# Performance work log

Hardware: AMD Instinct MI355X
Metric: run time of the kernel (lower is better)

Reference implementation:

```python
import jax, jax.numpy as jnp
import numpy as np

N_NODES = 100000
N_FEATS = 256
OUT_DIM = 64
NNZ_X = 1280000
N_EDGES = 1600000
KEEP_PROB = 0.9  # 1 - dropout_rate (dropout_rate = 0.1)


def setup_inputs() -> dict:
    key = jax.random.key(0)
    ks = jax.random.split(key, 7)
    feat_values = jax.random.normal(ks[0], (NNZ_X,), dtype=jnp.float32)
    feat_rows = jax.random.randint(ks[1], (NNZ_X,), 0, N_NODES, dtype=jnp.int32)
    feat_cols = jax.random.randint(ks[2], (NNZ_X,), 0, N_FEATS, dtype=jnp.int32)
    # GlorotNormal kernel: std = sqrt(2 / (fan_in + fan_out))
    glorot_std = float(np.sqrt(2.0 / (N_FEATS + OUT_DIM)))
    kernel = jax.random.normal(ks[3], (N_FEATS, OUT_DIM), dtype=jnp.float32) * glorot_std
    adj_values = jax.random.uniform(ks[4], (N_EDGES,), dtype=jnp.float32)
    adj_rows = jax.random.randint(ks[5], (N_EDGES,), 0, N_NODES, dtype=jnp.int32)
    adj_cols = jax.random.randint(ks[6], (N_EDGES,), 0, N_NODES, dtype=jnp.int32)
    return {
        "feat_values": feat_values,
        "kernel": kernel,
        "adj_values": adj_values,
        "feat_rows": feat_rows,
        "feat_cols": feat_cols,
        "adj_rows": adj_rows,
        "adj_cols": adj_cols,
    }


def reference(feat_values, kernel, adj_values, feat_rows, feat_cols, adj_rows, adj_cols):
    # sparse dropout on feature values (training=True path), deterministic key.
    # tf: keep = floor(keep_prob + U[0,1)) cast to bool; retain then scale 1/keep_prob
    u = jax.random.uniform(jax.random.key(42), feat_values.shape, dtype=feat_values.dtype)
    keep = jnp.floor(KEEP_PROB + u).astype(bool)
    v = jnp.where(keep, feat_values, jnp.zeros_like(feat_values)) * (1.0 / KEEP_PROB)

    # SpMM 1: XW[n, o] = sum_{(n,f) in X} v * kernel[f, o]
    xw = jax.ops.segment_sum(v[:, None] * kernel[feat_cols], feat_rows,
                             num_segments=N_NODES)  # [N, OUT]

    # SpMM 2: out[i, o] = sum_{(i,j) in A} a_ij * xw[j, o]
    agg = jax.ops.segment_sum(adj_values[:, None] * xw[adj_cols], adj_rows,
                              num_segments=N_NODES)  # [N, OUT]

    return jax.nn.relu(agg)
```

## Files before the change

### kernel.cpp

```cpp
#include <hip/hip_runtime.h>

#define N_NODES 100000
#define N_FEATS 256
#define OUT_DIM 64
#define NNZ_X   1280000
#define N_EDGES 1600000
#define NB      391
#define CHUNK   4096
#define KPT     8
#define CAPX    4352
#define CAPA    5120

__device__ __forceinline__ unsigned rotl32(unsigned x, unsigned d) {
    return (x << d) | (x >> (32u - d));
}

__device__ __forceinline__ float jax_uniform_42(unsigned e) {
    unsigned x0 = 0u, x1 = e;
    const unsigned ks0 = 0u, ks1 = 42u, ks2 = 0u ^ 42u ^ 0x1BD11BDAu;
    x0 += ks0; x1 += ks1;
#define TF_R(r) { x0 += x1; x1 = rotl32(x1, r); x1 ^= x0; }
    TF_R(13) TF_R(15) TF_R(26) TF_R(6)
    x0 += ks1; x1 += ks2 + 1u;
    TF_R(17) TF_R(29) TF_R(16) TF_R(24)
    x0 += ks2; x1 += ks0 + 2u;
    TF_R(13) TF_R(15) TF_R(26) TF_R(6)
    x0 += ks0; x1 += ks1 + 3u;
    TF_R(17) TF_R(29) TF_R(16) TF_R(24)
    x0 += ks1; x1 += ks2 + 4u;
    TF_R(13) TF_R(15) TF_R(26) TF_R(6)
    x0 += ks2; x1 += ks0 + 5u;
#undef TF_R
    unsigned bits = x0 ^ x1;
    return __uint_as_float((bits >> 9) | 0x3f800000u) - 1.0f;
}

__device__ __forceinline__ bool keep_42(unsigned e) {
    float u = jax_uniform_42(e);
    return floorf(0.9f + u) != 0.0f;
}

__device__ __forceinline__ unsigned short f32_bf16(float f) {
    unsigned bits = __float_as_uint(f);
    return (unsigned short)((bits + 0x7fffu + ((bits >> 16) & 1u)) >> 16);
}

__device__ __forceinline__ float bf16_f32(unsigned short u) {
    return __uint_as_float((unsigned)u << 16);
}

__global__ __launch_bounds__(512) void phase1(
        const float* __restrict__ fvals, const int* __restrict__ frows,
        const int* __restrict__ fcols,
        const float* __restrict__ avals, const int* __restrict__ arows,
        const int* __restrict__ acols,
        int* __restrict__ bcur_x, int* __restrict__ bcur_a,
        float2* __restrict__ gx, float2* __restrict__ ga) {
    const int isA = blockIdx.y;
    const float* vals = isA ? avals : fvals;
    const int* rows   = isA ? arows : frows;
    const int* cols   = isA ? acols : fcols;
    int* bcur         = isA ? bcur_a : bcur_x;
    float2* dst       = isA ? ga : gx;
    const unsigned cap = isA ? CAPA : CAPX;
    const unsigned n  = isA ? N_EDGES : NNZ_X;

    unsigned t = threadIdx.x;
    unsigned base = blockIdx.x * CHUNK;
    if (base >= n) return;

    __shared__ int cnt[512];
    __shared__ int start[512];
    __shared__ int cur[512];
    __shared__ int gbase[NB];
    __shared__ int s[256];
    __shared__ unsigned pArr[CHUNK];

    int rcache[KPT];

    cnt[t] = 0;
    __syncthreads();
    #pragma unroll
    for (int k = 0; k < KPT; k++) {
        unsigned i = base + k * 512u + t;
        int r = -1;
        if (i < n) {
            int rr = rows[i];
            if (isA || keep_42(i)) r = rr;
        }
        rcache[k] = r;
        if (r >= 0) atomicAdd(&cnt[(unsigned)r >> 8], 1);
    }
    __syncthreads();
    if (t < 256) s[t] = cnt[2*t] + cnt[2*t+1];
    __syncthreads();
    for (int off = 1; off < 256; off <<= 1) {
        int v = (t < 256u && t >= (unsigned)off) ? s[t - off] : 0;
        __syncthreads();
        if (t < 256u) s[t] += v;
        __syncthreads();
    }
    if (t < 256u) {
        int excl = t ? s[t-1] : 0;
        start[2*t]   = excl;
        start[2*t+1] = excl + cnt[2*t];
        cur[2*t]     = excl;
        cur[2*t+1]   = excl + cnt[2*t];
    }
    for (unsigned b = t; b < NB; b += 512u) {
        int cb = cnt[b];
        if (cb > 0) gbase[b] = atomicAdd(&bcur[b], cb);
    }
    __syncthreads();
    int n_valid = s[255];
    #pragma unroll
    for (int k = 0; k < KPT; k++) {
        int r = rcache[k];
        if (r >= 0) {
            unsigned b = (unsigned)r >> 8;
            int p = atomicAdd(&cur[b], 1);
            pArr[p] = (b << 20) | (((unsigned)r & 255u) << 12) | (k * 512u + t);
        }
    }
    __syncthreads();
    #pragma unroll
    for (int k = 0; k < KPT; k++) {
        int sidx = k * 512 + (int)t;
        if (sidx < n_valid) {
            unsigned m = pArr[sidx];
            unsigned b = m >> 20;
            unsigned rowlow = (m >> 12) & 255u;
            unsigned i = base + (m & 4095u);
            float v = vals[i];
            if (!isA) v *= (float)(1.0 / 0.9);
            unsigned packed = ((unsigned)cols[i] << 8) | rowlow;
            float2 e; e.x = v; e.y = __int_as_float((int)packed);
            dst[(size_t)b * cap + gbase[b] + (sidx - start[b])] = e;
        }
    }
}

__global__ __launch_bounds__(512) void sort_stage(
        const int* __restrict__ bcur_x, const float2* __restrict__ gx,
        const float* __restrict__ W, unsigned short* __restrict__ xw,
        const int* __restrict__ bcur_a, float2* __restrict__ ga,
        unsigned short* __restrict__ rs) {
    __shared__ float2 ent[CAPX];
    __shared__ int hist[256];
    __shared__ int starts[256];
    __shared__ int cursor[256];
    __shared__ int wtot[4];
    unsigned t = threadIdx.x;
    unsigned wid = t >> 6, lane = t & 63u;
    const int isA = (blockIdx.x >= NB);
    unsigned b = isA ? (blockIdx.x - NB) : blockIdx.x;

    if (!isA) {
        int cnt = bcur_x[b];
        const float2* src = gx + (size_t)b * CAPX;
        if (t < 256) hist[t] = 0;
        __syncthreads();
        for (int i = (int)t; i < cnt; i += 512)
            atomicAdd(&hist[((unsigned)__float_as_int(src[i].y)) & 255u], 1);
        __syncthreads();
        int inc = 0, binv = 0;
        if (wid < 4u) {
            unsigned bin = wid * 64u + lane;
            binv = hist[bin];
            inc = binv;
            #pragma unroll
            for (int d = 1; d < 64; d <<= 1) {
                int v = __shfl_up(inc, d, 64);
                if (lane >= (unsigned)d) inc += v;
            }
            if (lane == 63u) wtot[wid] = inc;
        }
        __syncthreads();
        if (wid < 4u) {
            int offw = 0;
            #pragma unroll
            for (int w = 0; w < 4; w++) if ((unsigned)w < wid) offw += wtot[w];
            unsigned bin = wid * 64u + lane;
            int excl = inc - binv + offw;
            starts[bin] = excl;
            cursor[bin] = excl;
        }
        __syncthreads();
        for (int i = (int)t; i < cnt; i += 512) {
            float2 e = src[i];
            int pos = atomicAdd(&cursor[((unsigned)__float_as_int(e.y)) & 255u], 1);
            ent[pos] = e;
        }
        __syncthreads();
        unsigned quarter = lane >> 4, sub = lane & 15u;
        const float4* W4 = (const float4*)W;
        ushort4* xw4 = (ushort4*)xw;
        for (unsigned r = wid; r < 256u; r += 8u) {
            int s0 = starts[r];
            int s1 = (r == 255u) ? cnt : starts[r + 1];
            float4 acc[4];
            #pragma unroll
            for (int j = 0; j < 4; j++) { acc[j].x = acc[j].y = acc[j].z = acc[j].w = 0.0f; }
            int p = s0;
            for (; p + 16 <= s1; p += 16) {
                float2 e[4];
                #pragma unroll
                for (int j = 0; j < 4; j++) e[j] = ent[p + 4 * quarter + j];
                float4 w[4];
                #pragma unroll
                for (int j = 0; j < 4; j++)
                    w[j] = W4[(((unsigned)__float_as_int(e[j].y)) >> 8) * 16u + sub];
                #pragma unroll
                for (int j = 0; j < 4; j++) {
                    acc[j].x = fmaf(e[j].x, w[j].x, acc[j].x);
                    acc[j].y = fmaf(e[j].x, w[j].y, acc[j].y);
                    acc[j].z = fmaf(e[j].x, w[j].z, acc[j].z);
                    acc[j].w = fmaf(e[j].x, w[j].w, acc[j].w);
                }
            }
            for (int q = p + (int)quarter; q < s1; q += 4) {
                float2 e = ent[q];
                float4 w = W4[(((unsigned)__float_as_int(e.y)) >> 8) * 16u + sub];
                acc[0].x = fmaf(e.x, w.x, acc[0].x);
                acc[0].y = fmaf(e.x, w.y, acc[0].y);
                acc[0].z = fmaf(e.x, w.z, acc[0].z);
                acc[0].w = fmaf(e.x, w.w, acc[0].w);
            }
            float ax = (acc[0].x + acc[1].x) + (acc[2].x + acc[3].x);
            float ay = (acc[0].y + acc[1].y) + (acc[2].y + acc[3].y);
            float az = (acc[0].z + acc[1].z) + (acc[2].z + acc[3].z);
            float aw = (acc[0].w + acc[1].w) + (acc[2].w + acc[3].w);
            ax += __shfl(ax, (int)(lane ^ 16u), 64);
            ay += __shfl(ay, (int)(lane ^ 16u), 64);
            az += __shfl(az, (int)(lane ^ 16u), 64);
            aw += __shfl(aw, (int)(lane ^ 16u), 64);
            ax += __shfl(ax, (int)(lane ^ 32u), 64);
            ay += __shfl(ay, (int)(lane ^ 32u), 64);
            az += __shfl(az, (int)(lane ^ 32u), 64);
            aw += __shfl(aw, (int)(lane ^ 32u), 64);
            unsigned grow = (b << 8) + r;
            if (quarter == 0 && grow < N_NODES) {
                ushort4 o;
                o.x = f32_bf16(ax); o.y = f32_bf16(ay);
                o.z = f32_bf16(az); o.w = f32_bf16(aw);
                xw4[(size_t)grow * 16u + sub] = o;
            }
        }
    } else {
        int cnt = bcur_a[b];
        float2* g = ga + (size_t)b * CAPA;
        if (t < 256) hist[t] = 0;
        __syncthreads();
        float2 ec[10];
        #pragma unroll
        for (int k = 0; k < 10; k++) {
            int i = k * 512 + (int)t;
            if (i < cnt) {
                float2 e = g[i];
                ec[k] = e;
                atomicAdd(&hist[((unsigned)__float_as_int(e.y)) & 255u], 1);
            }
        }
        __syncthreads();
        int inc = 0, binv = 0;
        if (wid < 4u) {
            unsigned bin = wid * 64u + lane;
            binv = hist[bin];
            inc = binv;
            #pragma unroll
            for (int d = 1; d < 64; d <<= 1) {
                int v = __shfl_up(inc, d, 64);
                if (lane >= (unsigned)d) inc += v;
            }
            if (lane == 63u) wtot[wid] = inc;
        }
        __syncthreads();
        if (wid < 4u) {
            int offw = 0;
            #pragma unroll
            for (int w = 0; w < 4; w++) if ((unsigned)w < wid) offw += wtot[w];
            unsigned bin = wid * 64u + lane;
            int excl = inc - binv + offw;
            cursor[bin] = excl;
            rs[(b << 8) + bin] = (unsigned short)excl;
        }
        __syncthreads();
        #pragma unroll
        for (int k = 0; k < 10; k++) {
            int i = k * 512 + (int)t;
            if (i < cnt) {
                unsigned packed = (unsigned)__float_as_int(ec[k].y);
                int pos = atomicAdd(&cursor[packed & 255u], 1);
                float2 o; o.x = ec[k].x; o.y = __int_as_float((int)(packed >> 8));
                g[pos] = o;
            }
        }
    }
}

__global__ void spmm2(const int* __restrict__ bcur_a,
                      const unsigned short* __restrict__ rs_a,
                      const float2* __restrict__ ga,
                      const unsigned short* __restrict__ xw,
                      float* __restrict__ out) {
    unsigned row  = blockIdx.x * 4u + (threadIdx.x >> 6);
    unsigned lane = threadIdx.x & 63u;
    if (row >= N_NODES) return;
    unsigned b = row >> 8, rl = row & 255u;
    int cnt = bcur_a[b];
    const float2* ent = ga + (size_t)b * CAPA;
    int s0 = rs_a[row];
    int s1 = (rl == 255u) ? cnt : (int)rs_a[row + 1];
    unsigned quarter = lane >> 4;
    unsigned sub     = lane & 15u;
    const ushort4* xw4 = (const ushort4*)xw;

    float4 acc[4];
    #pragma unroll
    for (int j = 0; j < 4; j++) { acc[j].x = acc[j].y = acc[j].z = acc[j].w = 0.0f; }
    int p = s0;
    for (; p + 16 <= s1; p += 16) {
        float2 e[4];
        #pragma unroll
        for (int j = 0; j < 4; j++) e[j] = ent[p + 4 * quarter + j];
        ushort4 u[4];
        #pragma unroll
        for (int j = 0; j < 4; j++)
            u[j] = xw4[((unsigned)__float_as_int(e[j].y)) * 16u + sub];
        #pragma unroll
        for (int j = 0; j < 4; j++) {
            acc[j].x = fmaf(e[j].x, bf16_f32(u[j].x), acc[j].x);
            acc[j].y = fmaf(e[j].x, bf16_f32(u[j].y), acc[j].y);
            acc[j].z = fmaf(e[j].x, bf16_f32(u[j].z), acc[j].z);
            acc[j].w = fmaf(e[j].x, bf16_f32(u[j].w), acc[j].w);
        }
    }
    for (int q = p + (int)quarter; q < s1; q += 4) {
        float2 e = ent[q];
        ushort4 u = xw4[((unsigned)__float_as_int(e.y)) * 16u + sub];
        acc[0].x = fmaf(e.x, bf16_f32(u.x), acc[0].x);
        acc[0].y = fmaf(e.x, bf16_f32(u.y), acc[0].y);
        acc[0].z = fmaf(e.x, bf16_f32(u.z), acc[0].z);
        acc[0].w = fmaf(e.x, bf16_f32(u.w), acc[0].w);
    }
    float ax = (acc[0].x + acc[1].x) + (acc[2].x + acc[3].x);
    float ay = (acc[0].y + acc[1].y) + (acc[2].y + acc[3].y);
    float az = (acc[0].z + acc[1].z) + (acc[2].z + acc[3].z);
    float aw = (acc[0].w + acc[1].w) + (acc[2].w + acc[3].w);
    ax += __shfl(ax, (int)(lane ^ 16u), 64);
    ay += __shfl(ay, (int)(lane ^ 16u), 64);
    az += __shfl(az, (int)(lane ^ 16u), 64);
    aw += __shfl(aw, (int)(lane ^ 16u), 64);
    ax += __shfl(ax, (int)(lane ^ 32u), 64);
    ay += __shfl(ay, (int)(lane ^ 32u), 64);
    az += __shfl(az, (int)(lane ^ 32u), 64);
    aw += __shfl(aw, (int)(lane ^ 32u), 64);
    if (quarter == 0) {
        float4 o;
        o.x = fmaxf(ax, 0.0f);
        o.y = fmaxf(ay, 0.0f);
        o.z = fmaxf(az, 0.0f);
        o.w = fmaxf(aw, 0.0f);
        ((float4*)out)[(size_t)row * 16u + sub] = o;
    }
}

extern "C" void kernel_launch(void* const* d_in, const int* in_sizes, int n_in,
                              void* d_out, int out_size, void* d_ws, size_t ws_size,
                              hipStream_t stream) {
    const float* feat_values = (const float*)d_in[0];
    const float* W           = (const float*)d_in[1];
    const float* adj_values  = (const float*)d_in[2];
    const int*   feat_rows   = (const int*)d_in[3];
    const int*   feat_cols   = (const int*)d_in[4];
    const int*   adj_rows    = (const int*)d_in[5];
    const int*   adj_cols    = (const int*)d_in[6];
    float* out = (float*)d_out;

    char* ws = (char*)d_ws;
    int* bcur_x = (int*)(ws + 0);
    int* bcur_a = (int*)(ws + 2048);
    unsigned short* rs_a = (unsigned short*)(ws + 4096);
    float2* gx  = (float2*)(ws + 204800);
    float2* ga  = (float2*)(ws + 13817856);
    unsigned short* xw = (unsigned short*)(ws + 29833216);

    hipMemsetAsync(ws, 0, 4096, stream);

    dim3 gp1((N_EDGES + CHUNK - 1) / CHUNK, 2);
    phase1<<<gp1, 512, 0, stream>>>(feat_values, feat_rows, feat_cols,
                                    adj_values, adj_rows, adj_cols,
                                    bcur_x, bcur_a, gx, ga);
    sort_stage<<<2 * NB, 512, 0, stream>>>(bcur_x, gx, W, xw, bcur_a, ga, rs_a);
    spmm2<<<(N_NODES + 3) / 4, 256, 0, stream>>>(bcur_a, rs_a, ga, xw, out);
}
```

Before: 209.7 us.

## Halve phase1 chunk, use wave-shuffle scan, process two rows per wave in spmm2

Phase1 now handles 2048 entries per block with 4 per thread and replaces the barrier-heavy shared-memory Hillis-Steele scan with a wave-level shuffle scan plus per-wave totals. The spmm2 kernel assigns two adjacent rows to each wavefront and interleaves their gathers, giving more independent loads in flight per wave. The intent is fewer block barriers and more memory-level parallelism. The cost is more blocks and global atomics in phase1, and higher register pressure and some load imbalance in spmm2.

```diff
diff --git a/kernel.cpp b/kernel.cpp
--- a/kernel.cpp
+++ b/kernel.cpp
@@ -6,8 +6,8 @@
 #define NNZ_X   1280000
 #define N_EDGES 1600000
 #define NB      391
-#define CHUNK   4096
-#define KPT     8
+#define CHUNK   2048
+#define KPT     4
 #define CAPX    4352
 #define CAPA    5120
 
@@ -66,6 +66,7 @@
     const unsigned n  = isA ? N_EDGES : NNZ_X;
 
     unsigned t = threadIdx.x;
+    unsigned wid = t >> 6, lane = t & 63u;
     unsigned base = blockIdx.x * CHUNK;
     if (base >= n) return;
 
@@ -73,7 +74,7 @@
     __shared__ int start[512];
     __shared__ int cur[512];
     __shared__ int gbase[NB];
-    __shared__ int s[256];
+    __shared__ int wtot[8];
     __shared__ unsigned pArr[CHUNK];
 
     int rcache[KPT];
@@ -92,27 +93,28 @@
         if (r >= 0) atomicAdd(&cnt[(unsigned)r >> 8], 1);
     }
     __syncthreads();
-    if (t < 256) s[t] = cnt[2*t] + cnt[2*t+1];
+    int binv = cnt[t];
+    int inc = binv;
+    #pragma unroll
+    for (int d = 1; d < 64; d <<= 1) {
+        int v = __shfl_up(inc, d, 64);
+        if (lane >= (unsigned)d) inc += v;
+    }
+    if (lane == 63u) wtot[wid] = inc;
     __syncthreads();
-    for (int off = 1; off < 256; off <<= 1) {
-        int v = (t < 256u && t >= (unsigned)off) ? s[t - off] : 0;
-        __syncthreads();
-        if (t < 256u) s[t] += v;
-        __syncthreads();
-    }
-    if (t < 256u) {
-        int excl = t ? s[t-1] : 0;
-        start[2*t]   = excl;
-        start[2*t+1] = excl + cnt[2*t];
-        cur[2*t]     = excl;
-        cur[2*t+1]   = excl + cnt[2*t];
-    }
-    for (unsigned b = t; b < NB; b += 512u) {
-        int cb = cnt[b];
-        if (cb > 0) gbase[b] = atomicAdd(&bcur[b], cb);
-    }
+    int offw = 0, total = 0;
+    #pragma unroll
+    for (int w = 0; w < 8; w++) {
+        int wv = wtot[w];
+        if ((unsigned)w < wid) offw += wv;
+        total += wv;
+    }
+    int excl = inc - binv + offw;
+    start[t] = excl;
+    cur[t]   = excl;
+    if (t < NB && binv > 0) gbase[t] = atomicAdd(&bcur[t], binv);
     __syncthreads();
-    int n_valid = s[255];
+    int n_valid = total;
     #pragma unroll
     for (int k = 0; k < KPT; k++) {
         int r = rcache[k];
@@ -130,7 +132,7 @@
             unsigned m = pArr[sidx];
             unsigned b = m >> 20;
             unsigned rowlow = (m >> 12) & 255u;
-            unsigned i = base + (m & 4095u);
+            unsigned i = base + (m & 2047u);
             float v = vals[i];
             if (!isA) v *= (float)(1.0 / 0.9);
             unsigned packed = ((unsigned)cols[i] << 8) | rowlow;
@@ -303,65 +305,137 @@
                       const float2* __restrict__ ga,
                       const unsigned short* __restrict__ xw,
                       float* __restrict__ out) {
-    unsigned row  = blockIdx.x * 4u + (threadIdx.x >> 6);
+    unsigned wid  = threadIdx.x >> 6;
     unsigned lane = threadIdx.x & 63u;
-    if (row >= N_NODES) return;
-    unsigned b = row >> 8, rl = row & 255u;
+    unsigned pair = blockIdx.x * 4u + wid;
+    unsigned row0 = pair * 2u;
+    if (row0 >= N_NODES) return;
+    unsigned row1 = row0 + 1u;
+    unsigned b = row0 >> 8;
     int cnt = bcur_a[b];
     const float2* ent = ga + (size_t)b * CAPA;
-    int s0 = rs_a[row];
-    int s1 = (rl == 255u) ? cnt : (int)rs_a[row + 1];
+    int s0a = rs_a[row0];
+    int s1a = rs_a[row1];
+    int s0b = s1a;
+    unsigned rl1 = row1 & 255u;
+    int s1b = (rl1 == 255u) ? cnt : (int)rs_a[row1 + 1];
     unsigned quarter = lane >> 4;
     unsigned sub     = lane & 15u;
     const ushort4* xw4 = (const ushort4*)xw;
 
-    float4 acc[4];
-    #pragma unroll
-    for (int j = 0; j < 4; j++) { acc[j].x = acc[j].y = acc[j].z = acc[j].w = 0.0f; }
-    int p = s0;
-    for (; p + 16 <= s1; p += 16) {
+    float4 accA[4], accB[4];
+    #pragma unroll
+    for (int j = 0; j < 4; j++) {
+        accA[j].x = accA[j].y = accA[j].z = accA[j].w = 0.0f;
+        accB[j].x = accB[j].y = accB[j].z = accB[j].w = 0.0f;
+    }
+    int pa = s0a, pb = s0b;
+    while (pa + 16 <= s1a && pb + 16 <= s1b) {
+        float2 ea[4], eb[4];
+        #pragma unroll
+        for (int j = 0; j < 4; j++) {
+            ea[j] = ent[pa + 4 * quarter + j];
+            eb[j] = ent[pb + 4 * quarter + j];
+        }
+        ushort4 ua[4], ub[4];
+        #pragma unroll
+        for (int j = 0; j < 4; j++) {
+            ua[j] = xw4[((unsigned)__float_as_int(ea[j].y)) * 16u + sub];
+            ub[j] = xw4[((unsigned)__float_as_int(eb[j].y)) * 16u + sub];
+        }
+        #pragma unroll
+        for (int j = 0; j < 4; j++) {
+            accA[j].x = fmaf(ea[j].x, bf16_f32(ua[j].x), accA[j].x);
+            accA[j].y = fmaf(ea[j].x, bf16_f32(ua[j].y), accA[j].y);
+            accA[j].z = fmaf(ea[j].x, bf16_f32(ua[j].z), accA[j].z);
+            accA[j].w = fmaf(ea[j].x, bf16_f32(ua[j].w), accA[j].w);
+            accB[j].x = fmaf(eb[j].x, bf16_f32(ub[j].x), accB[j].x);
+            accB[j].y = fmaf(eb[j].x, bf16_f32(ub[j].y), accB[j].y);
+            accB[j].z = fmaf(eb[j].x, bf16_f32(ub[j].z), accB[j].z);
+            accB[j].w = fmaf(eb[j].x, bf16_f32(ub[j].w), accB[j].w);
+        }
+        pa += 16; pb += 16;
+    }
+    for (; pa + 16 <= s1a; pa += 16) {
         float2 e[4];
         #pragma unroll
-        for (int j = 0; j < 4; j++) e[j] = ent[p + 4 * quarter + j];
+        for (int j = 0; j < 4; j++) e[j] = ent[pa + 4 * quarter + j];
         ushort4 u[4];
         #pragma unroll
         for (int j = 0; j < 4; j++)
             u[j] = xw4[((unsigned)__float_as_int(e[j].y)) * 16u + sub];
         #pragma unroll
         for (int j = 0; j < 4; j++) {
-            acc[j].x = fmaf(e[j].x, bf16_f32(u[j].x), acc[j].x);
-            acc[j].y = fmaf(e[j].x, bf16_f32(u[j].y), acc[j].y);
-            acc[j].z = fmaf(e[j].x, bf16_f32(u[j].z), acc[j].z);
-            acc[j].w = fmaf(e[j].x, bf16_f32(u[j].w), acc[j].w);
-        }
-    }
-    for (int q = p + (int)quarter; q < s1; q += 4) {
+            accA[j].x = fmaf(e[j].x, bf16_f32(u[j].x), accA[j].x);
+            accA[j].y = fmaf(e[j].x, bf16_f32(u[j].y), accA[j].y);
+            accA[j].z = fmaf(e[j].x, bf16_f32(u[j].z), accA[j].z);
+            accA[j].w = fmaf(e[j].x, bf16_f32(u[j].w), accA[j].w);
+        }
+    }
+    for (int q = pa + (int)quarter; q < s1a; q += 4) {
         float2 e = ent[q];
         ushort4 u = xw4[((unsigned)__float_as_int(e.y)) * 16u + sub];
-        acc[0].x = fmaf(e.x, bf16_f32(u.x), acc[0].x);
-        acc[0].y = fmaf(e.x, bf16_f32(u.y), acc[0].y);
-        acc[0].z = fmaf(e.x, bf16_f32(u.z), acc[0].z);
-        acc[0].w = fmaf(e.x, bf16_f32(u.w), acc[0].w);
-    }
-    float ax = (acc[0].x + acc[1].x) + (acc[2].x + acc[3].x);
-    float ay = (acc[0].y + acc[1].y) + (acc[2].y + acc[3].y);
-    float az = (acc[0].z + acc[1].z) + (acc[2].z + acc[3].z);
-    float aw = (acc[0].w + acc[1].w) + (acc[2].w + acc[3].w);
+        accA[0].x = fmaf(e.x, bf16_f32(u.x), accA[0].x);
+        accA[0].y = fmaf(e.x, bf16_f32(u.y), accA[0].y);
+        accA[0].z = fmaf(e.x, bf16_f32(u.z), accA[0].z);
+        accA[0].w = fmaf(e.x, bf16_f32(u.w), accA[0].w);
+    }
+    for (; pb + 16 <= s1b; pb += 16) {
+        float2 e[4];
+        #pragma unroll
+        for (int j = 0; j < 4; j++) e[j] = ent[pb + 4 * quarter + j];
+        ushort4 u[4];
+        #pragma unroll
+        for (int j = 0; j < 4; j++)
+            u[j] = xw4[((unsigned)__float_as_int(e[j].y)) * 16u + sub];
+        #pragma unroll
+        for (int j = 0; j < 4; j++) {
+            accB[j].x = fmaf(e[j].x, bf16_f32(u[j].x), accB[j].x);
+            accB[j].y = fmaf(e[j].x, bf16_f32(u[j].y), accB[j].y);
+            accB[j].z = fmaf(e[j].x, bf16_f32(u[j].z), accB[j].z);
+            accB[j].w = fmaf(e[j].x, bf16_f32(u[j].w), accB[j].w);
+        }
+    }
+    for (int q = pb + (int)quarter; q < s1b; q += 4) {
+        float2 e = ent[q];
+        ushort4 u = xw4[((unsigned)__float_as_int(e.y)) * 16u + sub];
+        accB[0].x = fmaf(e.x, bf16_f32(u.x), accB[0].x);
+        accB[0].y = fmaf(e.x, bf16_f32(u.y), accB[0].y);
+        accB[0].z = fmaf(e.x, bf16_f32(u.z), accB[0].z);
+        accB[0].w = fmaf(e.x, bf16_f32(u.w), accB[0].w);
+    }
+    float ax = (accA[0].x + accA[1].x) + (accA[2].x + accA[3].x);
+    float ay = (accA[0].y + accA[1].y) + (accA[2].y + accA[3].y);
+    float az = (accA[0].z + accA[1].z) + (accA[2].z + accA[3].z);
+    float aw = (accA[0].w + accA[1].w) + (accA[2].w + accA[3].w);
+    float bx = (accB[0].x + accB[1].x) + (accB[2].x + accB[3].x);
+    float by = (accB[0].y + accB[1].y) + (accB[2].y + accB[3].y);
+    float bz = (accB[0].z + accB[1].z) + (accB[2].z + accB[3].z);
+    float bw = (accB[0].w + accB[1].w) + (accB[2].w + accB[3].w);
     ax += __shfl(ax, (int)(lane ^ 16u), 64);
     ay += __shfl(ay, (int)(lane ^ 16u), 64);
     az += __shfl(az, (int)(lane ^ 16u), 64);
     aw += __shfl(aw, (int)(lane ^ 16u), 64);
+    bx += __shfl(bx, (int)(lane ^ 16u), 64);
+    by += __shfl(by, (int)(lane ^ 16u), 64);
+    bz += __shfl(bz, (int)(lane ^ 16u), 64);
+    bw += __shfl(bw, (int)(lane ^ 16u), 64);
     ax += __shfl(ax, (int)(lane ^ 32u), 64);
     ay += __shfl(ay, (int)(lane ^ 32u), 64);
     az += __shfl(az, (int)(lane ^ 32u), 64);
     aw += __shfl(aw, (int)(lane ^ 32u), 64);
+    bx += __shfl(bx, (int)(lane ^ 32u), 64);
+    by += __shfl(by, (int)(lane ^ 32u), 64);
+    bz += __shfl(bz, (int)(lane ^ 32u), 64);
+    bw += __shfl(bw, (int)(lane ^ 32u), 64);
     if (quarter == 0) {
-        float4 o;
-        o.x = fmaxf(ax, 0.0f);
-        o.y = fmaxf(ay, 0.0f);
-        o.z = fmaxf(az, 0.0f);
-        o.w = fmaxf(aw, 0.0f);
-        ((float4*)out)[(size_t)row * 16u + sub] = o;
+        float4 oa, ob;
+        oa.x = fmaxf(ax, 0.0f); oa.y = fmaxf(ay, 0.0f);
+        oa.z = fmaxf(az, 0.0f); oa.w = fmaxf(aw, 0.0f);
+        ob.x = fmaxf(bx, 0.0f); ob.y = fmaxf(by, 0.0f);
+        ob.z = fmaxf(bz, 0.0f); ob.w = fmaxf(bw, 0.0f);
+        ((float4*)out)[(size_t)row0 * 16u + sub] = oa;
+        ((float4*)out)[(size_t)row1 * 16u + sub] = ob;
     }
 }
 
@@ -392,5 +466,5 @@
                                     adj_values, adj_rows, adj_cols,
                                     bcur_x, bcur_a, gx, ga);
     sort_stage<<<2 * NB, 512, 0, stream>>>(bcur_x, gx, W, xw, bcur_a, ga, rs_a);
-    spmm2<<<(N_NODES + 3) / 4, 256, 0, stream>>>(bcur_a, rs_a, ga, xw, out);
-}
+    spmm2<<<(N_NODES / 2 + 3) / 4, 256, 0, stream>>>(bcur_a, rs_a, ga, xw, out);
+}
```

Result: slower. 214.9 us (+2.5%).
